# Performance work log

Measured on AMD Instinct MI355X. Metric: run time of the kernel, lower is better.

## Reference

```python
import jax, jax.numpy as jnp
import numpy as np

D = 4544
H = 71
DKV = 64  # D // H
NKV = 1   # multi-query: one shared KV head
ROPE_BASE = 10000.0


def setup_inputs() -> dict:
    key = jax.random.key(0)
    k1, k2, k3 = jax.random.split(key, 3)
    N, L = 2, 1024
    hidden_states = jax.random.normal(k1, (N, L, D), dtype=jnp.float32)
    W_qkv = jax.random.normal(k2, (D + 2 * NKV * DKV, D), dtype=jnp.float32) * (D ** -0.5)
    W_dense = jax.random.normal(k3, (D, D), dtype=jnp.float32) * (D ** -0.5)
    return {"hidden_states": hidden_states, "W_qkv": W_qkv, "W_dense": W_dense}


def _rope_cos_sin(L, dtype):
    inv_freq = 1.0 / (ROPE_BASE ** (jnp.arange(0, DKV, 2, dtype=jnp.float32) / DKV))  # [Dkv/2]
    t = jnp.arange(L, dtype=jnp.float32)
    freqs = jnp.outer(t, inv_freq)                 # [L, Dkv/2]
    emb = jnp.concatenate((freqs, freqs), axis=1)  # [L, Dkv]
    cos = jnp.cos(emb)[None, None, :, :].astype(dtype)  # [1,1,L,Dkv]
    sin = jnp.sin(emb)[None, None, :, :].astype(dtype)
    return cos, sin


def _rotate_half(x):
    half = x.shape[-1] // 2
    return jnp.concatenate((-x[..., half:], x[..., :half]), axis=-1)


def reference(hidden_states, W_qkv, W_dense):
    N, L, _ = hidden_states.shape
    # Fused QKV projection (no bias): [N, L, D + 2*Dkv]
    fused = jnp.einsum('nld,ed->nle', hidden_states, W_qkv)
    fused = fused.reshape(N, L, H + 2 * NKV, DKV)
    query = jnp.transpose(fused[:, :, : H, :], (0, 2, 1, 3))            # [N, H, L, Dkv]
    key_h = jnp.transpose(fused[:, :, H : H + NKV, :], (0, 2, 1, 3))    # [N, 1, L, Dkv]
    value = jnp.transpose(fused[:, :, H + NKV :, :], (0, 2, 1, 3))      # [N, 1, L, Dkv]

    # RoPE (prefill path: positions 0..L-1)
    cos, sin = _rope_cos_sin(L, query.dtype)
    query = query * cos + _rotate_half(query) * sin
    key_h = key_h * cos + _rotate_half(key_h) * sin

    # Causal SDPA with multi-query KV broadcast (scale = 1/sqrt(Dkv))
    k = key_h[:, 0]    # [N, L, Dkv]
    v = value[:, 0]    # [N, L, Dkv]
    scale = 1.0 / jnp.sqrt(jnp.asarray(DKV, dtype=query.dtype))
    scores = jnp.einsum('nhqd,nkd->nhqk', query, k) * scale  # [N, H, L, L]
    causal = jnp.tril(jnp.ones((L, L), dtype=bool))
    scores = jnp.where(causal[None, None], scores, jnp.finfo(scores.dtype).min)
    weights = jax.nn.softmax(scores, axis=-1)
    attn = jnp.einsum('nhqk,nkd->nhqd', weights, v)           # [N, H, L, Dkv]

    attn = jnp.transpose(attn, (0, 2, 1, 3)).reshape(N, L, H * DKV)  # [N, L, D]
    out = jnp.einsum('nld,ed->nle', attn, W_dense)
    return out
```

## Files before the change

kernel.cpp:

```cpp
#include <hip/hip_runtime.h>

#define D_MODEL 4544
#define E_QKV   4672
#define E_STR   4736
#define E_PAD2  4864
#define D_PAD   4608
#define NH      71
#define SEQ     1024
#define NB      2
#define M_ROWS  2048

typedef __bf16 bf16_t;
typedef bf16_t bf16x8 __attribute__((ext_vector_type(8)));
typedef float f32x4 __attribute__((ext_vector_type(4)));
typedef float f32x16 __attribute__((ext_vector_type(16)));
typedef unsigned u32x4 __attribute__((ext_vector_type(4)));

typedef __attribute__((address_space(1))) const void* gas_ptr;
typedef __attribute__((address_space(3))) void* las_ptr;

static __device__ __forceinline__ unsigned short f2bf(float f) {
  union { float f; unsigned u; } v; v.f = f;
  unsigned r = (v.u + 0x7fffu + ((v.u >> 16) & 1u)) >> 16;
  return (unsigned short)r;
}

static __device__ __forceinline__ unsigned cvtpk_bf16(float lo, float hi) {
  unsigned r;
  asm("v_cvt_pk_bf16_f32 %0, %1, %2" : "=v"(r) : "v"(lo), "v"(hi));
  return r;
}

static __device__ __forceinline__ float fast_exp2(float x) {
  float r;
  asm("v_exp_f32 %0, %1" : "=v"(r) : "v"(x));
  return r;
}

__global__ void convert_pad(const float* __restrict__ src, unsigned short* __restrict__ dst,
                            int rows_src, int rows_pad, int cols) {
  int idx = blockIdx.x * 256 + threadIdx.x;
  int cols4 = cols >> 2;
  int total = rows_pad * cols4;
  if (idx >= total) return;
  int row = idx / cols4;
  int c4 = (idx - row * cols4) << 2;
  ushort4 o;
  if (row < rows_src) {
    const float4 v = *(const float4*)(src + (size_t)row * cols + c4);
    o.x = f2bf(v.x); o.y = f2bf(v.y); o.z = f2bf(v.z); o.w = f2bf(v.w);
  } else {
    o.x = 0; o.y = 0; o.z = 0; o.w = 0;
  }
  *(ushort4*)(dst + (size_t)row * cols + c4) = o;
}

#define REGION(b_, op_, kh_) (((((b_)*2+(op_))*2)+(kh_)) << 13)

#define STAGE(b_, op_, kh_, kt_) do {                                          \
  const unsigned short* _src = (op_) ? B : A;                                  \
  const size_t _rb = (op_) ? bCol : bRow;                                      \
  _Pragma("unroll")                                                            \
  for (int _ld = 0; _ld < 2; ++_ld) {                                          \
    const int _fb = _ld * 8 + wave;                                            \
    const unsigned short* _ga = _src + (_rb + _fb * 16 + c) * K                \
                                + (kt_) * 64 + (kh_) * 32 + g * 8;             \
    __builtin_amdgcn_global_load_lds((gas_ptr)_ga,                             \
        (las_ptr)(lds + REGION(b_, op_, kh_) + (_fb << 9)), 16, 0, 0);         \
  }                                                                            \
} while (0)

#define LDA4(b_, kh_, mh_) do {                                                \
  const unsigned short* _ab = lds + REGION(b_, 0, kh_);                        \
  _Pragma("unroll")                                                            \
  for (int _mm = 0; _mm < 4; ++_mm)                                            \
    a[_mm] = *(const bf16x8*)&_ab[((wm * 8 + (mh_) * 4 + _mm) << 9) + lane * 8]; \
} while (0)

#define LDB4(b_, kh_) do {                                                     \
  const unsigned short* _bp = lds + REGION(b_, 1, kh_);                        \
  _Pragma("unroll")                                                            \
  for (int _n = 0; _n < 4; ++_n)                                               \
    bv[_n] = *(const bf16x8*)&_bp[((wn * 4 + _n) << 9) + lane * 8];            \
} while (0)

#define MFMA16(mh_) do {                                                       \
  _Pragma("unroll")                                                            \
  for (int _mm = 0; _mm < 4; ++_mm)                                            \
    _Pragma("unroll")                                                          \
    for (int _n = 0; _n < 4; ++_n)                                             \
      acc[(mh_) * 4 + _mm][_n] = __builtin_amdgcn_mfma_f32_16x16x32_bf16(      \
          a[_mm], bv[_n], acc[(mh_) * 4 + _mm][_n], 0, 0, 0);                  \
} while (0)

__global__ __launch_bounds__(512, 2) void gemm256(
    const unsigned short* __restrict__ A,
    const unsigned short* __restrict__ B,
    float* __restrict__ C0, float* __restrict__ C1, float* __restrict__ C2,
    int K, int Ntiles, int ldc, int Nact, int chunk) {
  __shared__ __align__(16) unsigned short lds[65536];
  const int tid = threadIdx.x;
  const int wave = tid >> 6, lane = tid & 63;
  const int g = lane >> 4, c = lane & 15;
  const int wm = wave >> 2, wn = wave & 3;
  const int nwg = gridDim.x;
  const int swz = (blockIdx.x & 7) * (nwg >> 3) + (blockIdx.x >> 3);
  const int tilesTot = 8 * Ntiles;
  const int kc = swz / tilesTot;
  const int tile = swz - kc * tilesTot;
  const int bm = tile / Ntiles, bn = tile - bm * Ntiles;
  const size_t bRow = (size_t)bm * 256, bCol = (size_t)bn * 256;
  const int NTtot = K >> 6;
  const int kb = kc * chunk;
  const int nt = (NTtot - kb < chunk) ? (NTtot - kb) : chunk;
  float* __restrict__ C = (kc == 0) ? C0 : ((kc == 1) ? C1 : C2);

  f32x4 acc[8][4] = {};

  STAGE(0, 0, 0, kb); STAGE(0, 1, 0, kb); STAGE(0, 0, 1, kb); STAGE(0, 1, 1, kb);
  STAGE(1, 1, 0, kb + 1); STAGE(1, 0, 0, kb + 1); STAGE(1, 1, 1, kb + 1);
  asm volatile("s_waitcnt vmcnt(6)" ::: "memory");
  __builtin_amdgcn_s_barrier();

  for (int t = 0; t < nt; ++t) {
    const int b = t & 1;
    const int tn1 = kb + ((t + 1 < nt) ? t + 1 : 0);
    const int tn2 = kb + ((t + 2 < nt) ? t + 2 : 0);
    bf16x8 a[4], bv[4];
    LDA4(b, 0, 0); LDB4(b, 0);
    STAGE(b ^ 1, 0, 1, tn1);
    __builtin_amdgcn_s_barrier();
    asm volatile("s_waitcnt lgkmcnt(0)" ::: "memory");
    __builtin_amdgcn_s_setprio(1);
    MFMA16(0);
    __builtin_amdgcn_s_setprio(0);
    __builtin_amdgcn_s_barrier();
    LDA4(b, 0, 1);
    STAGE(b, 1, 0, tn2);
    __builtin_amdgcn_s_barrier();
    asm volatile("s_waitcnt lgkmcnt(0)" ::: "memory");
    __builtin_amdgcn_s_setprio(1);
    MFMA16(1);
    __builtin_amdgcn_s_setprio(0);
    __builtin_amdgcn_s_barrier();
    LDA4(b, 1, 0); LDB4(b, 1);
    STAGE(b, 0, 0, tn2);
    __builtin_amdgcn_s_barrier();
    asm volatile("s_waitcnt lgkmcnt(0)" ::: "memory");
    __builtin_amdgcn_s_setprio(1);
    MFMA16(0);
    __builtin_amdgcn_s_setprio(0);
    __builtin_amdgcn_s_barrier();
    LDA4(b, 1, 1);
    STAGE(b, 1, 1, tn2);
    __builtin_amdgcn_s_barrier();
    asm volatile("s_waitcnt lgkmcnt(0)" ::: "memory");
    __builtin_amdgcn_s_setprio(1);
    MFMA16(1);
    __builtin_amdgcn_s_setprio(0);
    asm volatile("s_waitcnt vmcnt(6)" ::: "memory");
    __builtin_amdgcn_s_barrier();
  }
  asm volatile("s_waitcnt vmcnt(0)" ::: "memory");

#pragma unroll
  for (int mm = 0; mm < 8; ++mm) {
#pragma unroll
    for (int n = 0; n < 4; ++n) {
      int col = (int)bCol + wn * 64 + n * 16 + c;
      if (col < Nact) {
#pragma unroll
        for (int r = 0; r < 4; ++r) {
          size_t row = bRow + wm * 128 + mm * 16 + g * 4 + r;
          C[row * ldc + col] = acc[mm][n][r];
        }
      }
    }
  }
}

__global__ void reduce3(const float* __restrict__ p0, const float* __restrict__ p1,
                        const float* __restrict__ p2, float* __restrict__ out, int total4) {
  int idx = blockIdx.x * 256 + threadIdx.x;
  if (idx >= total4) return;
  float4 a = *(const float4*)(p0 + (size_t)idx * 4);
  float4 b = *(const float4*)(p1 + (size_t)idx * 4);
  float4 cc = *(const float4*)(p2 + (size_t)idx * 4);
  float4 o;
  o.x = a.x + b.x + cc.x; o.y = a.y + b.y + cc.y;
  o.z = a.z + b.z + cc.z; o.w = a.w + b.w + cc.w;
  *(float4*)(out + (size_t)idx * 4) = o;
}

__global__ void rope_extract(const float* __restrict__ p0, const float* __restrict__ p1,
                             const float* __restrict__ p2, int np,
                             unsigned short* __restrict__ Qb,
                             unsigned short* __restrict__ Kb,
                             unsigned short* __restrict__ VTb) {
  int idx = blockIdx.x * 256 + threadIdx.x;
  const int total = NB * SEQ * 73 * 64;
  if (idx >= total) return;
  int d = idx & 63;
  int t = idx >> 6;
  int h = t % 73;  t /= 73;
  int l = t & (SEQ - 1);
  int n = t >> 10;
  const size_t base = ((size_t)(n * SEQ + l)) * E_STR + h * 64;
  float x = p0[base + d];
  if (np == 3) x += p1[base + d] + p2[base + d];
  if (h == 72) {
    VTb[((size_t)(n * 64 + d)) * SEQ + l] = f2bf(x);
    return;
  }
  int dh = d & 31;
  float inv = __expf(-(float)dh * (9.210340371976184f / 32.0f));
  float ang = (float)l * inv;
  float sn, cs;
  __sincosf(ang, &sn, &cs);
  float xr0 = p0[base + ((d < 32) ? d + 32 : d - 32)];
  if (np == 3) xr0 += p1[base + ((d < 32) ? d + 32 : d - 32)] + p2[base + ((d < 32) ? d + 32 : d - 32)];
  float rh = (d < 32) ? -xr0 : xr0;
  float out = x * cs + rh * sn;
  if (h == 71) {
    Kb[((size_t)(n * SEQ + l)) * 64 + d] = f2bf(out);
  } else {
    Qb[(((size_t)(n * NH + h)) * SEQ + l) * 64 + d] = f2bf(out * 0.1803368801111204f);
  }
}

__global__ __launch_bounds__(128) void attn_kernel(
    const unsigned short* __restrict__ Qb,
    const unsigned short* __restrict__ Kb,
    const unsigned short* __restrict__ VTb,
    unsigned short* __restrict__ attnb) {
  const int h = blockIdx.y, n = blockIdx.z;
  const int wave = threadIdx.x >> 6, lane = threadIdx.x & 63;
  const int c = lane & 31, hi = lane >> 5;
  const int gw = blockIdx.x * 2 + wave;

  const unsigned short* kbase = Kb + (size_t)n * SEQ * 64;
  const unsigned short* vtbase = VTb + (size_t)n * 64 * SEQ;

  for (int pass = 0; pass < 2; ++pass) {
    const int tile = pass ? gw : (31 - gw);
    const int qrow0 = tile * 32;
    const int q = qrow0 + c;
    const unsigned short* qbase = Qb + (((size_t)(n * NH + h)) * SEQ + qrow0) * 64;

    bf16x8 qf[4];
#pragma unroll
    for (int cc = 0; cc < 4; ++cc)
      qf[cc] = *(const bf16x8*)&qbase[c * 64 + cc * 16 + hi * 8];

    f32x16 o0 = {}, o1 = {};
    float m_run = -1e30f, l_run = 0.f;

    for (int kt = 0; kt < qrow0 + 32; kt += 64) {
      f32x16 s0 = {}, s1 = {};
#pragma unroll
      for (int cc = 0; cc < 4; ++cc) {
        bf16x8 k0 = *(const bf16x8*)&kbase[(size_t)(kt + c) * 64 + cc * 16 + hi * 8];
        bf16x8 k1 = *(const bf16x8*)&kbase[(size_t)(kt + 32 + c) * 64 + cc * 16 + hi * 8];
        s0 = __builtin_amdgcn_mfma_f32_32x32x16_bf16(k0, qf[cc], s0, 0, 0, 0);
        s1 = __builtin_amdgcn_mfma_f32_32x32x16_bf16(k1, qf[cc], s1, 0, 0, 0);
      }
      if (kt + 63 > qrow0) {
#pragma unroll
        for (int r = 0; r < 16; ++r) {
          const int key0 = kt + (r & 3) + 8 * (r >> 2) + 4 * hi;
          s0[r] = (key0 > q) ? -1e30f : s0[r];
          s1[r] = (key0 + 32 > q) ? -1e30f : s1[r];
        }
      }
      float tt[16];
#pragma unroll
      for (int r = 0; r < 16; ++r) tt[r] = fmaxf(s0[r], s1[r]);
#pragma unroll
      for (int st = 8; st > 0; st >>= 1)
#pragma unroll
        for (int r = 0; r < 8; ++r) if (r < st) tt[r] = fmaxf(tt[r], tt[r + st]);
      float mx = fmaxf(tt[0], __shfl_xor(tt[0], 32));
      const float mnew = fmaxf(m_run, mx);
      const float aa = fast_exp2(m_run - mnew);
#pragma unroll
      for (int r = 0; r < 16; ++r) {
        s0[r] = fast_exp2(s0[r] - mnew);
        s1[r] = fast_exp2(s1[r] - mnew);
      }
      float ps = 0.f;
#pragma unroll
      for (int r = 0; r < 16; ++r) ps += s0[r] + s1[r];
      ps += __shfl_xor(ps, 32);
      l_run = l_run * aa + ps;
      m_run = mnew;
#pragma unroll
      for (int r = 0; r < 16; ++r) { o0[r] *= aa; o1[r] *= aa; }

#pragma unroll
      for (int half = 0; half < 2; ++half) {
#pragma unroll
        for (int ccl = 0; ccl < 2; ++ccl) {
          const int cg = half * 2 + ccl;
          unsigned a0, a1, b0, b1;
          if (half == 0) {
            a0 = cvtpk_bf16(s0[8 * ccl + 0], s0[8 * ccl + 1]);
            a1 = cvtpk_bf16(s0[8 * ccl + 2], s0[8 * ccl + 3]);
            b0 = cvtpk_bf16(s0[8 * ccl + 4], s0[8 * ccl + 5]);
            b1 = cvtpk_bf16(s0[8 * ccl + 6], s0[8 * ccl + 7]);
          } else {
            a0 = cvtpk_bf16(s1[8 * ccl + 0], s1[8 * ccl + 1]);
            a1 = cvtpk_bf16(s1[8 * ccl + 2], s1[8 * ccl + 3]);
            b0 = cvtpk_bf16(s1[8 * ccl + 4], s1[8 * ccl + 5]);
            b1 = cvtpk_bf16(s1[8 * ccl + 6], s1[8 * ccl + 7]);
          }
          unsigned xa0 = __shfl_xor(a0, 32), xa1 = __shfl_xor(a1, 32);
          unsigned xb0 = __shfl_xor(b0, 32), xb1 = __shfl_xor(b1, 32);
          u32x4 fw;
          fw[0] = hi ? xb0 : a0;
          fw[1] = hi ? xb1 : a1;
          fw[2] = hi ? b0 : xa0;
          fw[3] = hi ? b1 : xa1;
          union { u32x4 u; bf16x8 b; } pf; pf.u = fw;
          bf16x8 v0 = *(const bf16x8*)&vtbase[(size_t)c * SEQ + kt + cg * 16 + hi * 8];
          bf16x8 v1 = *(const bf16x8*)&vtbase[(size_t)(32 + c) * SEQ + kt + cg * 16 + hi * 8];
          o0 = __builtin_amdgcn_mfma_f32_32x32x16_bf16(v0, pf.b, o0, 0, 0, 0);
          o1 = __builtin_amdgcn_mfma_f32_32x32x16_bf16(v1, pf.b, o1, 0, 0, 0);
        }
      }
    }

    const float inv = 1.0f / l_run;
    const size_t rowoff = (size_t)(n * SEQ + q) * D_MODEL + h * 64;
#pragma unroll
    for (int rr = 0; rr < 4; ++rr) {
      ushort4 w0, w1;
      w0.x = f2bf(o0[4 * rr + 0] * inv); w0.y = f2bf(o0[4 * rr + 1] * inv);
      w0.z = f2bf(o0[4 * rr + 2] * inv); w0.w = f2bf(o0[4 * rr + 3] * inv);
      w1.x = f2bf(o1[4 * rr + 0] * inv); w1.y = f2bf(o1[4 * rr + 1] * inv);
      w1.z = f2bf(o1[4 * rr + 2] * inv); w1.w = f2bf(o1[4 * rr + 3] * inv);
      *(ushort4*)&attnb[rowoff + 8 * rr + 4 * hi] = w0;
      *(ushort4*)&attnb[rowoff + 32 + 8 * rr + 4 * hi] = w1;
    }
  }
}

extern "C" void kernel_launch(void* const* d_in, const int* in_sizes, int n_in,
                              void* d_out, int out_size, void* d_ws, size_t ws_size,
                              hipStream_t stream) {
  const float* hs = (const float*)d_in[0];
  const float* wqkv = (const float*)d_in[1];
  const float* wdense = (const float*)d_in[2];
  float* out = (float*)d_out;
  char* ws = (char*)d_ws;

  unsigned short* hsb   = (unsigned short*)(ws + 0);
  unsigned short* wqkvb = (unsigned short*)(ws + 18612224);
  unsigned short* wdb   = (unsigned short*)(ws + 62820352);
  float*          fused = (float*)(ws + 104701952);
  unsigned short* qb    = (unsigned short*)(ws + 143499264);
  unsigned short* kb    = (unsigned short*)(ws + 162111488);
  unsigned short* vtb   = (unsigned short*)(ws + 162373632);
  unsigned short* attnb = (unsigned short*)(ws + 162635776);
  float* fusedE1 = (float*)(ws + 181248000);
  float* fusedE2 = (float*)(ws + 220045312);
  const int splitOK = (ws_size >= (size_t)258842624) ? 1 : 0;

  {
    int total = M_ROWS * (D_MODEL / 4);
    convert_pad<<<(total + 255) / 256, 256, 0, stream>>>(hs, hsb, M_ROWS, M_ROWS, D_MODEL);
  }
  {
    int total = E_PAD2 * (D_MODEL / 4);
    convert_pad<<<(total + 255) / 256, 256, 0, stream>>>(wqkv, wqkvb, E_QKV, E_PAD2, D_MODEL);
  }
  {
    int total = D_PAD * (D_MODEL / 4);
    convert_pad<<<(total + 255) / 256, 256, 0, stream>>>(wdense, wdb, D_MODEL, D_PAD, D_MODEL);
  }

  if (splitOK) {
    gemm256<<<dim3(8 * 19 * 3), 512, 0, stream>>>(hsb, wqkvb, fused, fusedE1, fusedE2,
                                                  D_MODEL, 19, E_STR, E_STR, 24);
  } else {
    gemm256<<<dim3(8 * 19), 512, 0, stream>>>(hsb, wqkvb, fused, fused, fused,
                                              D_MODEL, 19, E_STR, E_STR, 71);
  }
  {
    int total = NB * SEQ * 73 * 64;
    rope_extract<<<(total + 255) / 256, 256, 0, stream>>>(fused, fusedE1, fusedE2,
                                                          splitOK ? 3 : 1, qb, kb, vtb);
  }
  attn_kernel<<<dim3(8, NH, NB), 128, 0, stream>>>(qb, kb, vtb, attnb);
  if (splitOK) {
    float* p0 = (float*)(ws + 0);
    float* p1 = fused;
    float* p2 = fusedE1;
    gemm256<<<dim3(8 * 18 * 3), 512, 0, stream>>>(attnb, wdb, p0, p1, p2,
                                                  D_MODEL, 18, D_MODEL, D_MODEL, 24);
    int total4 = (M_ROWS * D_MODEL) / 4;
    reduce3<<<(total4 + 255) / 256, 256, 0, stream>>>(p0, p1, p2, out, total4);
  } else {
    gemm256<<<dim3(8 * 18), 512, 0, stream>>>(attnb, wdb, out, out, out,
                                              D_MODEL, 18, D_MODEL, D_MODEL, 71);
  }
}
```

Measured before the change: 433.2 us.

## Restructure GEMM main loop into two superphases with fewer barriers

The GEMM inner loop goes from four phases, each with two barriers and a full LDS wait, to two superphases. Each superphase loads both M-halves of A fragments plus the B fragments, issues two global-to-LDS stages, and uses a partial lgkmcnt wait so the second MFMA batch's loads overlap the first batch. Per-thread global base pointers are hoisted out of the STAGE macro to cut address arithmetic, and the RoPE kernel's index computation is tidied. This halves barrier count per K-tile, at the cost of more live registers and a changed prefetch ordering that depends on the vmcnt counts being right.

New measurement: 445.2 us. +2.8%, slower.

```diff
diff --git a/kernel.cpp b/kernel.cpp
--- a/kernel.cpp
+++ b/kernel.cpp
@@ -58,39 +58,56 @@
 #define REGION(b_, op_, kh_) (((((b_)*2+(op_))*2)+(kh_)) << 13)
 
 #define STAGE(b_, op_, kh_, kt_) do {                                          \
-  const unsigned short* _src = (op_) ? B : A;                                  \
-  const size_t _rb = (op_) ? bCol : bRow;                                      \
-  _Pragma("unroll")                                                            \
-  for (int _ld = 0; _ld < 2; ++_ld) {                                          \
-    const int _fb = _ld * 8 + wave;                                            \
-    const unsigned short* _ga = _src + (_rb + _fb * 16 + c) * K                \
-                                + (kt_) * 64 + (kh_) * 32 + g * 8;             \
-    __builtin_amdgcn_global_load_lds((gas_ptr)_ga,                             \
-        (las_ptr)(lds + REGION(b_, op_, kh_) + (_fb << 9)), 16, 0, 0);         \
-  }                                                                            \
+  const unsigned short* _p0 = (op_) ? pB0 : pA0;                               \
+  const unsigned short* _p1 = (op_) ? pB1 : pA1;                               \
+  const int _koff = ((kt_) << 6) + ((kh_) << 5);                               \
+  __builtin_amdgcn_global_load_lds((gas_ptr)(_p0 + _koff),                     \
+      (las_ptr)(lds + REGION(b_, op_, kh_) + (wave << 9)), 16, 0, 0);          \
+  __builtin_amdgcn_global_load_lds((gas_ptr)(_p1 + _koff),                     \
+      (las_ptr)(lds + REGION(b_, op_, kh_) + ((8 + wave) << 9)), 16, 0, 0);    \
 } while (0)
 
-#define LDA4(b_, kh_, mh_) do {                                                \
+#define LDA4G(dst_, b_, kh_, mh_) do {                                         \
   const unsigned short* _ab = lds + REGION(b_, 0, kh_);                        \
   _Pragma("unroll")                                                            \
   for (int _mm = 0; _mm < 4; ++_mm)                                            \
-    a[_mm] = *(const bf16x8*)&_ab[((wm * 8 + (mh_) * 4 + _mm) << 9) + lane * 8]; \
+    dst_[_mm] = *(const bf16x8*)&_ab[((wm * 8 + (mh_) * 4 + _mm) << 9) + lane * 8]; \
 } while (0)
 
-#define LDB4(b_, kh_) do {                                                     \
+#define LDB4G(dst_, b_, kh_) do {                                              \
   const unsigned short* _bp = lds + REGION(b_, 1, kh_);                        \
   _Pragma("unroll")                                                            \
   for (int _n = 0; _n < 4; ++_n)                                               \
-    bv[_n] = *(const bf16x8*)&_bp[((wn * 4 + _n) << 9) + lane * 8];            \
+    dst_[_n] = *(const bf16x8*)&_bp[((wn * 4 + _n) << 9) + lane * 8];          \
 } while (0)
 
-#define MFMA16(mh_) do {                                                       \
+#define MFMA16G(af_, bf_, mh_) do {                                            \
   _Pragma("unroll")                                                            \
   for (int _mm = 0; _mm < 4; ++_mm)                                            \
     _Pragma("unroll")                                                          \
     for (int _n = 0; _n < 4; ++_n)                                             \
       acc[(mh_) * 4 + _mm][_n] = __builtin_amdgcn_mfma_f32_16x16x32_bf16(      \
-          a[_mm], bv[_n], acc[(mh_) * 4 + _mm][_n], 0, 0, 0);                  \
+          af_[_mm], bf_[_n], acc[(mh_) * 4 + _mm][_n], 0, 0, 0);               \
+} while (0)
+
+#define SUPERPHASE(b_, kh_, SB_, VW_) do {                                     \
+  bf16x8 aL[4], aH[4], bv[4];                                                  \
+  LDA4G(aL, b_, kh_, 0); LDB4G(bv, b_, kh_);                                   \
+  __builtin_amdgcn_sched_barrier(0);                                           \
+  LDA4G(aH, b_, kh_, 1);                                                       \
+  __builtin_amdgcn_sched_barrier(0);                                           \
+  SB_;                                                                         \
+  __builtin_amdgcn_s_barrier();                                                \
+  asm volatile("s_waitcnt lgkmcnt(4)" ::: "memory");                           \
+  __builtin_amdgcn_sched_barrier(0);                                           \
+  __builtin_amdgcn_s_setprio(1);                                               \
+  MFMA16G(aL, bv, 0);                                                          \
+  asm volatile("s_waitcnt lgkmcnt(0)" ::: "memory");                           \
+  __builtin_amdgcn_sched_barrier(0);                                           \
+  MFMA16G(aH, bv, 1);                                                          \
+  __builtin_amdgcn_s_setprio(0);                                               \
+  VW_;                                                                         \
+  __builtin_amdgcn_s_barrier();                                                \
 } while (0)
 
 __global__ __launch_bounds__(512, 2) void gemm256(
@@ -115,51 +132,28 @@
   const int nt = (NTtot - kb < chunk) ? (NTtot - kb) : chunk;
   float* __restrict__ C = (kc == 0) ? C0 : ((kc == 1) ? C1 : C2);
 
+  const unsigned short* pA0 = A + (bRow + (size_t)(wave * 16 + c)) * K + g * 8;
+  const unsigned short* pA1 = A + (bRow + (size_t)((8 + wave) * 16 + c)) * K + g * 8;
+  const unsigned short* pB0 = B + (bCol + (size_t)(wave * 16 + c)) * K + g * 8;
+  const unsigned short* pB1 = B + (bCol + (size_t)((8 + wave) * 16 + c)) * K + g * 8;
+
   f32x4 acc[8][4] = {};
 
   STAGE(0, 0, 0, kb); STAGE(0, 1, 0, kb); STAGE(0, 0, 1, kb); STAGE(0, 1, 1, kb);
-  STAGE(1, 1, 0, kb + 1); STAGE(1, 0, 0, kb + 1); STAGE(1, 1, 1, kb + 1);
-  asm volatile("s_waitcnt vmcnt(6)" ::: "memory");
+  STAGE(1, 0, 0, kb + 1); STAGE(1, 1, 0, kb + 1);
+  asm volatile("s_waitcnt vmcnt(4)" ::: "memory");
   __builtin_amdgcn_s_barrier();
 
   for (int t = 0; t < nt; ++t) {
     const int b = t & 1;
     const int tn1 = kb + ((t + 1 < nt) ? t + 1 : 0);
     const int tn2 = kb + ((t + 2 < nt) ? t + 2 : 0);
-    bf16x8 a[4], bv[4];
-    LDA4(b, 0, 0); LDB4(b, 0);
-    STAGE(b ^ 1, 0, 1, tn1);
-    __builtin_amdgcn_s_barrier();
-    asm volatile("s_waitcnt lgkmcnt(0)" ::: "memory");
-    __builtin_amdgcn_s_setprio(1);
-    MFMA16(0);
-    __builtin_amdgcn_s_setprio(0);
-    __builtin_amdgcn_s_barrier();
-    LDA4(b, 0, 1);
-    STAGE(b, 1, 0, tn2);
-    __builtin_amdgcn_s_barrier();
-    asm volatile("s_waitcnt lgkmcnt(0)" ::: "memory");
-    __builtin_amdgcn_s_setprio(1);
-    MFMA16(1);
-    __builtin_amdgcn_s_setprio(0);
-    __builtin_amdgcn_s_barrier();
-    LDA4(b, 1, 0); LDB4(b, 1);
-    STAGE(b, 0, 0, tn2);
-    __builtin_amdgcn_s_barrier();
-    asm volatile("s_waitcnt lgkmcnt(0)" ::: "memory");
-    __builtin_amdgcn_s_setprio(1);
-    MFMA16(0);
-    __builtin_amdgcn_s_setprio(0);
-    __builtin_amdgcn_s_barrier();
-    LDA4(b, 1, 1);
-    STAGE(b, 1, 1, tn2);
-    __builtin_amdgcn_s_barrier();
-    asm volatile("s_waitcnt lgkmcnt(0)" ::: "memory");
-    __builtin_amdgcn_s_setprio(1);
-    MFMA16(1);
-    __builtin_amdgcn_s_setprio(0);
-    asm volatile("s_waitcnt vmcnt(6)" ::: "memory");
-    __builtin_amdgcn_s_barrier();
+    SUPERPHASE(b, 0,
+               { STAGE(b ^ 1, 0, 1, tn1); STAGE(b ^ 1, 1, 1, tn1); },
+               {});
+    SUPERPHASE(b, 1,
+               { STAGE(b, 0, 0, tn2); STAGE(b, 1, 0, tn2); },
+               { asm volatile("s_waitcnt vmcnt(4)" ::: "memory"); });
   }
   asm volatile("s_waitcnt vmcnt(0)" ::: "memory");
 
@@ -217,9 +211,10 @@
   float ang = (float)l * inv;
   float sn, cs;
   __sincosf(ang, &sn, &cs);
-  float xr0 = p0[base + ((d < 32) ? d + 32 : d - 32)];
-  if (np == 3) xr0 += p1[base + ((d < 32) ? d + 32 : d - 32)] + p2[base + ((d < 32) ? d + 32 : d - 32)];
-  float rh = (d < 32) ? -xr0 : xr0;
+  int dx = (d < 32) ? d + 32 : d - 32;
+  float xr = p0[base + dx];
+  if (np == 3) xr += p1[base + dx] + p2[base + dx];
+  float rh = (d < 32) ? -xr : xr;
   float out = x * cs + rh * sn;
   if (h == 71) {
     Kb[((size_t)(n * SEQ + l)) * 64 + d] = f2bf(out);
```

## Prefetch next K tile and hoist V loads in attention kernel loop

Applied to the files above, without the earlier changes.

The attention kernel now loads the K fragments for the next 64-key tile into registers while the current tile's QK MFMAs and softmax run, and issues all V loads for the tile ahead of the softmax, fenced by a sched_barrier. This is meant to hide global load latency behind compute. The GEMM staging macro now uses per-thread base pointers computed once, which removes repeated address arithmetic. The RoPE kernel's rotated-index expression is also cleaned up. Holding extra K and V fragments in registers raises VGPR pressure and may lower occupancy.

Measured after the change: 433.1 us. No clear change (-0.0%).

```diff
diff --git a/kernel.cpp b/kernel.cpp
--- a/kernel.cpp
+++ b/kernel.cpp
@@ -58,16 +58,13 @@
 #define REGION(b_, op_, kh_) (((((b_)*2+(op_))*2)+(kh_)) << 13)
 
 #define STAGE(b_, op_, kh_, kt_) do {                                          \
-  const unsigned short* _src = (op_) ? B : A;                                  \
-  const size_t _rb = (op_) ? bCol : bRow;                                      \
-  _Pragma("unroll")                                                            \
-  for (int _ld = 0; _ld < 2; ++_ld) {                                          \
-    const int _fb = _ld * 8 + wave;                                            \
-    const unsigned short* _ga = _src + (_rb + _fb * 16 + c) * K                \
-                                + (kt_) * 64 + (kh_) * 32 + g * 8;             \
-    __builtin_amdgcn_global_load_lds((gas_ptr)_ga,                             \
-        (las_ptr)(lds + REGION(b_, op_, kh_) + (_fb << 9)), 16, 0, 0);         \
-  }                                                                            \
+  const unsigned short* _p0 = (op_) ? pB0 : pA0;                               \
+  const unsigned short* _p1 = (op_) ? pB1 : pA1;                               \
+  const int _koff = ((kt_) << 6) + ((kh_) << 5);                               \
+  __builtin_amdgcn_global_load_lds((gas_ptr)(_p0 + _koff),                     \
+      (las_ptr)(lds + REGION(b_, op_, kh_) + (wave << 9)), 16, 0, 0);          \
+  __builtin_amdgcn_global_load_lds((gas_ptr)(_p1 + _koff),                     \
+      (las_ptr)(lds + REGION(b_, op_, kh_) + ((8 + wave) << 9)), 16, 0, 0);    \
 } while (0)
 
 #define LDA4(b_, kh_, mh_) do {                                                \
@@ -115,6 +112,11 @@
   const int nt = (NTtot - kb < chunk) ? (NTtot - kb) : chunk;
   float* __restrict__ C = (kc == 0) ? C0 : ((kc == 1) ? C1 : C2);
 
+  const unsigned short* pA0 = A + (bRow + (size_t)(wave * 16 + c)) * K + g * 8;
+  const unsigned short* pA1 = A + (bRow + (size_t)((8 + wave) * 16 + c)) * K + g * 8;
+  const unsigned short* pB0 = B + (bCol + (size_t)(wave * 16 + c)) * K + g * 8;
+  const unsigned short* pB1 = B + (bCol + (size_t)((8 + wave) * 16 + c)) * K + g * 8;
+
   f32x4 acc[8][4] = {};
 
   STAGE(0, 0, 0, kb); STAGE(0, 1, 0, kb); STAGE(0, 0, 1, kb); STAGE(0, 1, 1, kb);
@@ -217,9 +219,10 @@
   float ang = (float)l * inv;
   float sn, cs;
   __sincosf(ang, &sn, &cs);
-  float xr0 = p0[base + ((d < 32) ? d + 32 : d - 32)];
-  if (np == 3) xr0 += p1[base + ((d < 32) ? d + 32 : d - 32)] + p2[base + ((d < 32) ? d + 32 : d - 32)];
-  float rh = (d < 32) ? -xr0 : xr0;
+  int dx = (d < 32) ? d + 32 : d - 32;
+  float xr = p0[base + dx];
+  if (np == 3) xr += p1[base + dx] + p2[base + dx];
+  float rh = (d < 32) ? -xr : xr;
   float out = x * cs + rh * sn;
   if (h == 71) {
     Kb[((size_t)(n * SEQ + l)) * 64 + d] = f2bf(out);
@@ -227,6 +230,14 @@
     Qb[(((size_t)(n * NH + h)) * SEQ + l) * 64 + d] = f2bf(out * 0.1803368801111204f);
   }
 }
+
+#define LOADK(dst_, ktv_) do {                                                 \
+  _Pragma("unroll")                                                            \
+  for (int _cc = 0; _cc < 4; ++_cc) {                                          \
+    dst_[_cc]     = *(const bf16x8*)&kbase[(size_t)((ktv_) + c) * 64 + _cc * 16 + hi * 8];      \
+    dst_[4 + _cc] = *(const bf16x8*)&kbase[(size_t)((ktv_) + 32 + c) * 64 + _cc * 16 + hi * 8]; \
+  }                                                                            \
+} while (0)
 
 __global__ __launch_bounds__(128) void attn_kernel(
     const unsigned short* __restrict__ Qb,
@@ -245,6 +256,7 @@
     const int tile = pass ? gw : (31 - gw);
     const int qrow0 = tile * 32;
     const int q = qrow0 + c;
+    const int nk = qrow0 + 32;
     const unsigned short* qbase = Qb + (((size_t)(n * NH + h)) * SEQ + qrow0) * 64;
 
     bf16x8 qf[4];
@@ -255,15 +267,25 @@
     f32x16 o0 = {}, o1 = {};
     float m_run = -1e30f, l_run = 0.f;
 
-    for (int kt = 0; kt < qrow0 + 32; kt += 64) {
+    bf16x8 kc[8], kn[8];
+    LOADK(kc, 0);
+
+    for (int kt = 0; kt < nk; kt += 64) {
+      const bool more = (kt + 64) < nk;
       f32x16 s0 = {}, s1 = {};
 #pragma unroll
       for (int cc = 0; cc < 4; ++cc) {
-        bf16x8 k0 = *(const bf16x8*)&kbase[(size_t)(kt + c) * 64 + cc * 16 + hi * 8];
-        bf16x8 k1 = *(const bf16x8*)&kbase[(size_t)(kt + 32 + c) * 64 + cc * 16 + hi * 8];
-        s0 = __builtin_amdgcn_mfma_f32_32x32x16_bf16(k0, qf[cc], s0, 0, 0, 0);
-        s1 = __builtin_amdgcn_mfma_f32_32x32x16_bf16(k1, qf[cc], s1, 0, 0, 0);
-      }
+        s0 = __builtin_amdgcn_mfma_f32_32x32x16_bf16(kc[cc], qf[cc], s0, 0, 0, 0);
+        s1 = __builtin_amdgcn_mfma_f32_32x32x16_bf16(kc[4 + cc], qf[cc], s1, 0, 0, 0);
+      }
+      if (more) LOADK(kn, kt + 64);
+      bf16x8 vv0[4], vv1[4];
+#pragma unroll
+      for (int cg = 0; cg < 4; ++cg) {
+        vv0[cg] = *(const bf16x8*)&vtbase[(size_t)c * SEQ + kt + cg * 16 + hi * 8];
+        vv1[cg] = *(const bf16x8*)&vtbase[(size_t)(32 + c) * SEQ + kt + cg * 16 + hi * 8];
+      }
+      __builtin_amdgcn_sched_barrier(0);
       if (kt + 63 > qrow0) {
 #pragma unroll
         for (int r = 0; r < 16; ++r) {
@@ -321,11 +343,13 @@
           fw[2] = hi ? b0 : xa0;
           fw[3] = hi ? b1 : xa1;
           union { u32x4 u; bf16x8 b; } pf; pf.u = fw;
-          bf16x8 v0 = *(const bf16x8*)&vtbase[(size_t)c * SEQ + kt + cg * 16 + hi * 8];
-          bf16x8 v1 = *(const bf16x8*)&vtbase[(size_t)(32 + c) * SEQ + kt + cg * 16 + hi * 8];
-          o0 = __builtin_amdgcn_mfma_f32_32x32x16_bf16(v0, pf.b, o0, 0, 0, 0);
-          o1 = __builtin_amdgcn_mfma_f32_32x32x16_bf16(v1, pf.b, o1, 0, 0, 0);
+          o0 = __builtin_amdgcn_mfma_f32_32x32x16_bf16(vv0[cg], pf.b, o0, 0, 0, 0);
+          o1 = __builtin_amdgcn_mfma_f32_32x32x16_bf16(vv1[cg], pf.b, o1, 0, 0, 0);
         }
+      }
+      if (more) {
+#pragma unroll
+        for (int cc = 0; cc < 8; ++cc) kc[cc] = kn[cc];
       }
     }
 
```
